# Performance work log

Hardware: AMD Instinct MI355X
Metric: run time of the kernel (lower is better)

The kernel has to match this reference:

```python
import jax, jax.numpy as jnp
import numpy as np

H = 32  # rnn/encoder/residual hidden dim
NEG = -1e9


def gru(x, h0, Wih, Whh, bih, bhh):
    # x: (B,T,D), h0: (B,H); torch GRU gate order [r,z,n]
    xp = jnp.swapaxes(x @ Wih.T + bih, 0, 1)  # (T,B,3H)

    def step(h, xt):
        gh = h @ Whh.T + bhh
        xr, xz, xn = jnp.split(xt, 3, axis=-1)
        hr, hz, hn = jnp.split(gh, 3, axis=-1)
        r = jax.nn.sigmoid(xr + hr)
        z = jax.nn.sigmoid(xz + hz)
        n = jnp.tanh(xn + r * hn)
        h_new = (1.0 - z) * n + z * h
        return h_new, h_new

    hT, ys = jax.lax.scan(step, h0, xp)
    return jnp.swapaxes(ys, 0, 1), hT  # (B,T,H), (B,H)


def setup_inputs():
    key = jax.random.key(0)
    ks = jax.random.split(key, 30)
    B, T = 2048, 128
    def lin(k, o, i):
        return jax.random.normal(k, (o, i), jnp.float32) / np.sqrt(i)
    inp = {}
    inp['obs'] = jax.random.normal(ks[0], (B, T, 15), jnp.float32)
    inp['rnn_state'] = jax.random.normal(ks[1], (1, B, 3 * H), jnp.float32)
    inp['enc_air_W'] = lin(ks[2], H, 7); inp['enc_air_b'] = jnp.zeros((H,), jnp.float32)
    inp['enc_m_W'] = lin(ks[3], H, 4); inp['enc_m_b'] = jnp.zeros((H,), jnp.float32)
    inp['air_Wih'] = lin(ks[4], 3 * H, H); inp['air_Whh'] = lin(ks[5], 3 * H, H)
    inp['air_bih'] = jnp.zeros((3 * H,), jnp.float32); inp['air_bhh'] = jnp.zeros((3 * H,), jnp.float32)
    inp['m_Wih'] = lin(ks[6], 3 * H, H); inp['m_Whh'] = lin(ks[7], 3 * H, H)
    inp['m_bih'] = jnp.zeros((3 * H,), jnp.float32); inp['m_bhh'] = jnp.zeros((3 * H,), jnp.float32)
    inp['attn_in_w'] = lin(ks[8], 3 * H, H); inp['attn_in_b'] = jnp.zeros((3 * H,), jnp.float32)
    inp['attn_out_w'] = lin(ks[9], H, H); inp['attn_out_b'] = jnp.zeros((H,), jnp.float32)
    inp['mlp_W0'] = lin(ks[10], 256, 2 * H); inp['mlp_b0'] = jnp.zeros((256,), jnp.float32)
    inp['mlp_W1'] = lin(ks[11], 256, 256); inp['mlp_b1'] = jnp.zeros((256,), jnp.float32)
    inp['out_W'] = lin(ks[12], 1, 256); inp['out_b'] = jnp.zeros((1,), jnp.float32)
    return inp


def reference(obs, rnn_state, enc_air_W, enc_air_b, enc_m_W, enc_m_b,
              air_Wih, air_Whh, air_bih, air_bhh,
              m_Wih, m_Whh, m_bih, m_bhh,
              attn_in_w, attn_in_b, attn_out_w, attn_out_b,
              mlp_W0, mlp_b0, mlp_W1, mlp_b1, out_W, out_b):
    B, T, _ = obs.shape
    h_air0 = rnn_state[0, :, :H]                       # (B,H)
    h_m0 = rnn_state[0, :, H:].reshape(2 * B, H)       # faithful reshape (1,B,64)->(1,2B,32)

    # aircraft branch
    air_emb = obs[..., 8:] @ enc_air_W.T + enc_air_b   # (B,T,H)
    air_feat, next_h_air = gru(air_emb, h_air0, air_Wih, air_Whh, air_bih, air_bhh)

    # missile branch: concat missiles along batch dim
    m_raw = jnp.concatenate([obs[..., 0:4], obs[..., 4:8]], axis=0)  # (2B,T,4)
    m_emb = m_raw @ enc_m_W.T + enc_m_b
    m_feat, next_h_m = gru(m_emb, h_m0, m_Wih, m_Whh, m_bih, m_bhh)
    m1_feat, m2_feat = m_feat[:B], m_feat[B:]

    # inactive-missile mask from raw obs
    obs_flat = obs.reshape(-1, 15)
    inact = jnp.array([1.0, 0.0, 1.0, 0.0], jnp.float32)
    mask = jnp.stack([
        jnp.all(jnp.isclose(obs_flat[:, 0:4], inact), axis=-1),
        jnp.all(jnp.isclose(obs_flat[:, 4:8], inact), axis=-1),
    ], axis=1)                                          # (N,2) True = masked

    N = B * T
    air_flat = air_feat.reshape(N, H)
    m1_flat = m1_feat.reshape(N, H)
    m2_flat = m2_feat.reshape(N, H)

    # 2-head attention, q len 1, kv len 2
    Wq, Wk, Wv = jnp.split(attn_in_w, 3, axis=0)
    bq, bk, bv = jnp.split(attn_in_b, 3, axis=0)
    nh, hd = 2, H // 2
    qh = (air_flat @ Wq.T + bq).reshape(N, nh, hd)
    kv = jnp.stack([m1_flat, m2_flat], axis=1)          # (N,2,H)
    kh = (kv @ Wk.T + bk).reshape(N, 2, nh, hd)
    vh = (kv @ Wv.T + bv).reshape(N, 2, nh, hd)
    scores = jnp.einsum('nhd,nkhd->nhk', qh, kh) / np.sqrt(hd)
    scores = scores + jnp.where(mask[:, None, :], NEG, 0.0)
    w = jax.nn.softmax(scores, axis=-1)
    ctx = jnp.einsum('nhk,nkhd->nhd', w, vh).reshape(N, H)
    attn = ctx @ attn_out_w.T + attn_out_b
    attn = jnp.where(jnp.all(mask, axis=-1, keepdims=True), 0.0, attn)  # torch nan_to_num(all-masked)

    fusion = jnp.concatenate([air_flat, attn], axis=-1)  # (N,2H)
    h1 = jax.nn.leaky_relu(fusion @ mlp_W0.T + mlp_b0, 0.01)
    h2 = jax.nn.leaky_relu(h1 @ mlp_W1.T + mlp_b1, 0.01)
    val = h2 @ out_W.T + out_b                           # (N,1)

    next_h = jnp.concatenate([next_h_air, next_h_m.reshape(B, 2 * H)], axis=-1)[None]  # (1,B,96)
    return val, next_h
```

## Files before the change

kernel.cpp:

```cpp
#include <hip/hip_runtime.h>
#include <hip/hip_bf16.h>

#define BB 2048
#define TT 128
#define NN (BB*TT)
#define NVAL NN

#define OFF_W0P   2048u
#define OFF_W1P   10240u
#define OFF_WQKV  43008u
#define OFF_WO    44544u
#define OFF_PWHA  49792u
#define OFF_PWHM  51328u
#define OFF_PWCA  52864u
#define OFF_PWCM  54400u
#define OFF_BHNA  55936u
#define OFF_BHNM  55968u
#define OFF_AIRF  83968u
#define OFF_MF    4278272u
#define OFF_MASK  12666880u

typedef __attribute__((ext_vector_type(8))) short short8;
typedef __attribute__((ext_vector_type(4))) float f32x4;
typedef _Float16 f16x8 __attribute__((ext_vector_type(8)));
typedef unsigned u32x4 __attribute__((ext_vector_type(4)));

__device__ __forceinline__ unsigned short f2bf(float f) {
    unsigned u = __builtin_bit_cast(unsigned, f);
    u += 0x7FFFu + ((u >> 16) & 1u);
    return (unsigned short)(u >> 16);
}
__device__ __forceinline__ unsigned f2h(float f) {
    _Float16 h = (_Float16)f;
    return (unsigned)__builtin_bit_cast(unsigned short, h);
}
__device__ __forceinline__ unsigned pkh2(float a, float b) {
    return (f2h(b) << 16) | f2h(a);
}
__device__ __forceinline__ float fast_rcp(float x) {
    return __builtin_amdgcn_rcpf(x);
}
__device__ __forceinline__ unsigned cvt_pk_bf16(float a, float b) {
    unsigned r;
    asm("v_cvt_pk_bf16_f32 %0, %1, %2" : "=v"(r) : "v"(a), "v"(b));
    return r;
}
__device__ __forceinline__ f32x4 mfma16f(f16x8 a, f16x8 b, f32x4 c) {
    return __builtin_amdgcn_mfma_f32_16x16x32_f16(a, b, c, 0, 0, 0);
}

__global__ __launch_bounds__(256) void prep_kernel(
    const float* __restrict__ enc_air_W, const float* __restrict__ enc_air_b,
    const float* __restrict__ enc_m_W,   const float* __restrict__ enc_m_b,
    const float* __restrict__ air_Wih,   const float* __restrict__ air_bih,
    const float* __restrict__ m_Wih,     const float* __restrict__ m_bih,
    const float* __restrict__ air_Whh,   const float* __restrict__ m_Whh,
    const float* __restrict__ air_bhh,   const float* __restrict__ m_bhh,
    const float* __restrict__ W0,        const float* __restrict__ W1,
    const float* __restrict__ attn_in_w, const float* __restrict__ attn_out_w,
    float* __restrict__ ws)
{
    int b = blockIdx.x, t = threadIdx.x;
    if (b == 0) {
    } else if (b <= 32) {
        unsigned short* w1p = (unsigned short*)(ws + OFF_W1P);
        int base = ((b-1)*256 + t);
        int lane = base & 63;
        int ctf  = base >> 6;
        int ct   = ctf & 15, s = ctf >> 4;
        int col = lane & 15, quad = lane >> 4;
        int k0 = s*32 + quad*8;
        int o  = ct*16 + col;
        #pragma unroll
        for (int j = 0; j < 8; j++)
            w1p[base*8 + j] = f2bf(W1[o*256 + k0 + j]);
    } else if (b <= 40) {
        unsigned short* w0p = (unsigned short*)(ws + OFF_W0P);
        int base = ((b-33)*256 + t);
        int lane = base & 63;
        int ctf  = base >> 6;
        int ct   = ctf & 15, s = ctf >> 4;
        int col = lane & 15, quad = lane >> 4;
        int k0 = s*32 + quad*8;
        int o  = ct*16 + col;
        #pragma unroll
        for (int j = 0; j < 8; j++)
            w0p[base*8 + j] = f2bf(W0[o*64 + k0 + j]);
    } else if (b == 41) {
        unsigned short* wqkv = (unsigned short*)(ws + OFF_WQKV);
        unsigned short* wop  = (unsigned short*)(ws + OFF_WO);
        for (int slot = t; slot < 512; slot += 256) {
            if (slot < 384) {
                int ct = slot >> 6, lane = slot & 63;
                int col = lane & 15, quad = lane >> 4;
                int o = ct*16 + col;
                #pragma unroll
                for (int j = 0; j < 8; j++)
                    wqkv[slot*8 + j] = f2bf(attn_in_w[o*32 + quad*8 + j]);
            } else {
                int s2 = slot - 384;
                int ct = s2 >> 6, lane = s2 & 63;
                int col = lane & 15, quad = lane >> 4;
                #pragma unroll
                for (int j = 0; j < 8; j++)
                    wop[s2*8 + j] = f2bf(attn_out_w[(ct*16+col)*32 + quad*8 + j]);
            }
        }
    } else if (b == 42) {
        unsigned* pa = (unsigned*)(ws + OFF_PWHA);
        unsigned* pm = (unsigned*)(ws + OFF_PWHM);
        for (int s = t; s < 3072; s += 256) {
            int s2 = (s < 1536) ? s : s - 1536;
            const float* W = (s < 1536) ? air_Whh : m_Whh;
            unsigned* dst = (s < 1536) ? pa : pm;
            int tile = s2 >> 8;
            int l    = (s2 >> 2) & 63;
            int d    = s2 & 3;
            int gate = tile >> 1, hfp = tile & 1;
            int rr = l & 15;
            int f  = (rr >> 2)*8 + hfp*4 + (rr & 3);
            int k  = (l >> 4)*8 + d*2;
            int row = gate*32 + f;
            dst[s2] = pkh2(W[row*32 + k], W[row*32 + k + 1]);
        }
    } else {
        unsigned* pa = (unsigned*)(ws + OFF_PWCA);
        unsigned* pm = (unsigned*)(ws + OFF_PWCM);
        for (int s = t; s < 3072; s += 256) {
            bool isA = (s < 1536);
            int s2 = isA ? s : s - 1536;
            unsigned* dst = isA ? pa : pm;
            int tile = s2 >> 8, l = (s2 >> 2) & 63, d = s2 & 3;
            int gate = tile >> 1, hfp = tile & 1;
            int rr = l & 15;
            int f = (rr >> 2)*8 + hfp*4 + (rr & 3);
            int o = gate*32 + f;
            int kb = (l >> 4)*8 + d*2;
            int ni = isA ? 7 : 4;
            float v[2];
            #pragma unroll
            for (int e = 0; e < 2; e++) {
                int k = kb + e;
                float acc = 0.f;
                if (k < ni) {
                    for (int m = 0; m < 32; m++)
                        acc += isA ? air_Wih[o*32+m]*enc_air_W[m*7+k]
                                   : m_Wih[o*32+m]*enc_m_W[m*4+k];
                } else if (k == ni) {
                    acc = isA ? air_bih[o] : m_bih[o];
                    for (int m = 0; m < 32; m++)
                        acc += isA ? air_Wih[o*32+m]*enc_air_b[m]
                                   : m_Wih[o*32+m]*enc_m_b[m];
                    if (gate < 2) acc += isA ? air_bhh[o] : m_bhh[o];
                }
                v[e] = acc;
            }
            dst[s2] = pkh2(v[0], v[1]);
        }
        if (t < 32) {
            ws[OFF_BHNA + t] = air_bhh[64 + t];
            ws[OFF_BHNM + t] = m_bhh[64 + t];
        }
    }
}

template<bool AIRT>
__device__ __forceinline__ void gru_tile(
    const float* __restrict__ obs, const float* __restrict__ rnn,
    const float* __restrict__ ws,
    unsigned short* __restrict__ feat, float* __restrict__ mask_f,
    float* __restrict__ nh_out, int tileIdx)
{
    const int lane = threadIdx.x & 63;
    const int col = lane & 15, quad = lane >> 4;
    const bool q0 = (quad == 0);

    const unsigned* pw = (const unsigned*)(ws + (AIRT ? OFF_PWHA : OFF_PWHM));
    const unsigned* pc = (const unsigned*)(ws + (AIRT ? OFF_PWCA : OFF_PWCM));
    f16x8 whf[6], wcf[6];
    #pragma unroll
    for (int i6 = 0; i6 < 6; i6++) {
        whf[i6] = __builtin_bit_cast(f16x8, *(const u32x4*)(pw + i6*256 + lane*4));
        wcf[i6] = __builtin_bit_cast(f16x8, *(const u32x4*)(pc + i6*256 + lane*4));
    }
    const float* bhnp = ws + (AIRT ? OFF_BHNA : OFF_BHNM) + quad*8;
    f32x4 bhn0 = *(const f32x4*)(bhnp);
    f32x4 bhn1 = *(const f32x4*)(bhnp + 4);

    int hbase, brow = 0, slot = 0;
    size_t featOff;
    const float* xptr;
    if (AIRT) {
        int r = tileIdx*16 + col;
        hbase = r*96;
        featOff = (size_t)r*(TT*32);
        xptr = obs + (size_t)r*(TT*15) + 8;
    } else {
        int i = tileIdx*16 + col;
        slot = (i >= BB) ? 1 : 0;
        brow = i - slot*BB;
        hbase = (i >> 1)*96 + 32 + (i & 1)*32;
        featOff = (size_t)i*(TT*32);
        xptr = obs + (size_t)brow*(TT*15) + slot*4;
    }
    unsigned short* featp = feat + featOff + quad*8;

    f32x4 h0v = *(const f32x4*)(rnn + hbase + quad*8);
    f32x4 h1v = *(const f32x4*)(rnn + hbase + quad*8 + 4);

    constexpr int NI = AIRT ? 7 : 4;
    float nx[NI];
    #pragma unroll
    for (int u = 0; u < NI; u++) nx[u] = xptr[u];

    #pragma unroll 1
    for (int t = 0; t < TT; t++) {
        float cx[NI];
        #pragma unroll
        for (int u = 0; u < NI; u++) cx[u] = nx[u];
        const int tn = (t < TT-1) ? (t+1)*15 : t*15;
        #pragma unroll
        for (int u = 0; u < NI; u++) nx[u] = xptr[tn + u];

        if (!AIRT) {
            bool ok = (fabsf(cx[0] - 1.f) <= 1.00001e-5f) &&
                      (fabsf(cx[1])       <= 1e-8f) &&
                      (fabsf(cx[2] - 1.f) <= 1.00001e-5f) &&
                      (fabsf(cx[3])       <= 1e-8f);
            if (q0) mask_f[((size_t)brow*TT + t)*2 + slot] = ok ? 1.f : 0.f;
        }

        unsigned xd0, xd1, xd2, xd3;
        if (AIRT) {
            xd0 = pkh2(cx[0], cx[1]); xd1 = pkh2(cx[2], cx[3]);
            xd2 = pkh2(cx[4], cx[5]); xd3 = pkh2(cx[6], 1.0f);
        } else {
            xd0 = pkh2(cx[0], cx[1]); xd1 = pkh2(cx[2], cx[3]);
            xd2 = 0x00003C00u;        xd3 = 0u;
        }
        u32x4 xdv;
        xdv[0] = q0 ? xd0 : 0u; xdv[1] = q0 ? xd1 : 0u;
        xdv[2] = q0 ? xd2 : 0u; xdv[3] = q0 ? xd3 : 0u;
        f16x8 xf = __builtin_bit_cast(f16x8, xdv);

        u32x4 hdv;
        hdv[0] = pkh2(h0v[0], h0v[1]); hdv[1] = pkh2(h0v[2], h0v[3]);
        hdv[2] = pkh2(h1v[0], h1v[1]); hdv[3] = pkh2(h1v[2], h1v[3]);
        f16x8 hff = __builtin_bit_cast(f16x8, hdv);

        const f32x4 z4 = {0.f, 0.f, 0.f, 0.f};
        f32x4 aR0 = mfma16f(whf[0], hff, mfma16f(wcf[0], xf, z4));
        f32x4 aR1 = mfma16f(whf[1], hff, mfma16f(wcf[1], xf, z4));
        f32x4 aZ0 = mfma16f(whf[2], hff, mfma16f(wcf[2], xf, z4));
        f32x4 aZ1 = mfma16f(whf[3], hff, mfma16f(wcf[3], xf, z4));
        f32x4 aXN0 = mfma16f(wcf[4], xf, z4);
        f32x4 aXN1 = mfma16f(wcf[5], xf, z4);
        f32x4 aHN0 = mfma16f(whf[4], hff, z4);
        f32x4 aHN1 = mfma16f(whf[5], hff, z4);

        #pragma unroll
        for (int s = 0; s < 4; s++) {
            {
                float r  = fast_rcp(1.f + __expf(-aR0[s]));
                float z  = fast_rcp(1.f + __expf(-aZ0[s]));
                float hn = aHN0[s] + bhn0[s];
                float pre = aXN0[s] + r*hn;
                float e2 = __expf(2.f*pre);
                float n  = 1.f - 2.f*fast_rcp(e2 + 1.f);
                h0v[s] = n + z*(h0v[s] - n);
            }
            {
                float r  = fast_rcp(1.f + __expf(-aR1[s]));
                float z  = fast_rcp(1.f + __expf(-aZ1[s]));
                float hn = aHN1[s] + bhn1[s];
                float pre = aXN1[s] + r*hn;
                float e2 = __expf(2.f*pre);
                float n  = 1.f - 2.f*fast_rcp(e2 + 1.f);
                h1v[s] = n + z*(h1v[s] - n);
            }
        }

        u32x4 fw;
        fw[0] = cvt_pk_bf16(h0v[0], h0v[1]); fw[1] = cvt_pk_bf16(h0v[2], h0v[3]);
        fw[2] = cvt_pk_bf16(h1v[0], h1v[1]); fw[3] = cvt_pk_bf16(h1v[2], h1v[3]);
        *(u32x4*)(featp + (size_t)t*32) = fw;
    }
    *(f32x4*)(nh_out + hbase + quad*8)     = h0v;
    *(f32x4*)(nh_out + hbase + quad*8 + 4) = h1v;
}

__global__ __launch_bounds__(64) void gru_kernel(
    const float* __restrict__ obs, const float* __restrict__ rnn,
    const float* __restrict__ ws,
    unsigned short* __restrict__ air_feat, unsigned short* __restrict__ m_feat,
    float* __restrict__ mask_f, float* __restrict__ nh_out)
{
    int g = blockIdx.x;
    if (g < 128) gru_tile<true >(obs, rnn, ws, air_feat, mask_f, nh_out, g);
    else         gru_tile<false>(obs, rnn, ws, m_feat,  mask_f, nh_out, g - 128);
}

__global__ __launch_bounds__(256) void fused_kernel(
    const unsigned short* __restrict__ air_feat, const unsigned short* __restrict__ m_feat,
    const float* __restrict__ mask_f,
    const unsigned short* __restrict__ wqkv, const float* __restrict__ attn_in_b,
    const unsigned short* __restrict__ wop,  const float* __restrict__ attn_out_b,
    const unsigned short* __restrict__ w0p, const float* __restrict__ b0,
    const unsigned short* __restrict__ w1p, const float* __restrict__ b1,
    const float* __restrict__ outW, const float* __restrict__ outb,
    float* __restrict__ val)
{
    __shared__ unsigned short A1[64*72];
    __shared__ unsigned short U[64*264];
    __shared__ float MS[128];
    __shared__ float PS[4][64];

    unsigned short* AM = U;
    unsigned short* CT = U + 64*72;
    unsigned short* A2 = U;

    const int tid  = threadIdx.x;
    const int lane = tid & 63;
    const int strip = tid >> 6;
    const int col  = lane & 15;
    const int quad = lane >> 4;
    const size_t n0 = (size_t)blockIdx.x * 64;

    short8 wqf[2], wkf[2], wvf[2], wof[2];
    #pragma unroll
    for (int ct = 0; ct < 2; ct++) {
        wqf[ct] = *(const short8*)(wqkv + ((0+ct)*64 + lane)*8);
        wkf[ct] = *(const short8*)(wqkv + ((2+ct)*64 + lane)*8);
        wvf[ct] = *(const short8*)(wqkv + ((4+ct)*64 + lane)*8);
        wof[ct] = *(const short8*)(wop + (ct*64 + lane)*8);
    }

    {
        int row = tid >> 2, c0 = (tid & 3)*8;
        short8 va  = *(const short8*)(air_feat + (n0 + row)*32 + c0);
        *(short8*)&A1[row*72 + c0] = va;
        short8 vm1 = *(const short8*)(m_feat + (n0 + row)*32 + c0);
        *(short8*)&AM[row*72 + c0] = vm1;
        short8 vm2 = *(const short8*)(m_feat + ((size_t)NN + n0 + row)*32 + c0);
        *(short8*)&AM[row*72 + 32 + c0] = vm2;
        if (tid < 128) MS[tid] = mask_f[n0*2 + tid];
    }
    __syncthreads();

    {
        short8 a_air = *(const short8*)&A1[(strip*16 + col)*72 + quad*8];
        short8 a_m1  = *(const short8*)&AM[(strip*16 + col)*72 + quad*8];
        short8 a_m2  = *(const short8*)&AM[(strip*16 + col)*72 + 32 + quad*8];

        f32x4 q[2], k1[2], k2[2], v1[2], v2[2], ao[2];
        #pragma unroll
        for (int ct = 0; ct < 2; ct++) {
            f32x4 z = (f32x4){0.f,0.f,0.f,0.f};
            q[ct]  = __builtin_amdgcn_mfma_f32_16x16x32_bf16(a_air, wqf[ct], z, 0,0,0);
            k1[ct] = __builtin_amdgcn_mfma_f32_16x16x32_bf16(a_m1,  wkf[ct], z, 0,0,0);
            k2[ct] = __builtin_amdgcn_mfma_f32_16x16x32_bf16(a_m2,  wkf[ct], z, 0,0,0);
            v1[ct] = __builtin_amdgcn_mfma_f32_16x16x32_bf16(a_m1,  wvf[ct], z, 0,0,0);
            v2[ct] = __builtin_amdgcn_mfma_f32_16x16x32_bf16(a_m2,  wvf[ct], z, 0,0,0);
        }
        float bqr[2], bkr[2], bvr[2];
        #pragma unroll
        for (int ct = 0; ct < 2; ct++) {
            bqr[ct] = attn_in_b[ct*16 + col];
            bkr[ct] = attn_in_b[32 + ct*16 + col];
            bvr[ct] = attn_in_b[64 + ct*16 + col];
        }
        float p1s[2][4], p2s[2][4];
        #pragma unroll
        for (int ct = 0; ct < 2; ct++) {
            #pragma unroll
            for (int reg = 0; reg < 4; reg++) {
                float qq = q[ct][reg] + bqr[ct];
                float p1 = qq * (k1[ct][reg] + bkr[ct]);
                float p2 = qq * (k2[ct][reg] + bkr[ct]);
                #pragma unroll
                for (int m = 1; m < 16; m <<= 1) {
                    p1 += __shfl_xor(p1, m, 64);
                    p2 += __shfl_xor(p2, m, 64);
                }
                p1s[ct][reg] = p1; p2s[ct][reg] = p2;
            }
        }
        float bothm[4];
        #pragma unroll
        for (int reg = 0; reg < 4; reg++) {
            int rloc = strip*16 + quad*4 + reg;
            float m0v = MS[rloc*2], m1v = MS[rloc*2 + 1];
            bothm[reg] = (m0v > 0.5f && m1v > 0.5f) ? 1.f : 0.f;
            #pragma unroll
            for (int ct = 0; ct < 2; ct++) {
                float s1 = p1s[ct][reg]*0.25f + (m0v > 0.5f ? -1e9f : 0.f);
                float s2 = p2s[ct][reg]*0.25f + (m1v > 0.5f ? -1e9f : 0.f);
                float mx = fmaxf(s1, s2);
                float e1 = __expf(s1 - mx), e2 = __expf(s2 - mx);
                float inv = fast_rcp(e1 + e2);
                float ctxv = ((v1[ct][reg] + bvr[ct])*e1 +
                              (v2[ct][reg] + bvr[ct])*e2) * inv;
                CT[rloc*40 + ct*16 + col] = f2bf(ctxv);
            }
        }
        short8 a_ctx = *(const short8*)&CT[(strip*16 + col)*40 + quad*8];
        #pragma unroll
        for (int ct = 0; ct < 2; ct++) {
            f32x4 z = (f32x4){0.f,0.f,0.f,0.f};
            ao[ct] = __builtin_amdgcn_mfma_f32_16x16x32_bf16(a_ctx, wof[ct], z, 0,0,0);
        }
        float bor[2] = { attn_out_b[col], attn_out_b[16 + col] };
        #pragma unroll
        for (int reg = 0; reg < 4; reg++) {
            int rloc = strip*16 + quad*4 + reg;
            #pragma unroll
            for (int ct = 0; ct < 2; ct++) {
                float av = ao[ct][reg] + bor[ct];
                av = (bothm[reg] > 0.5f) ? 0.f : av;
                A1[rloc*72 + 32 + ct*16 + col] = f2bf(av);
            }
        }
    }
    __syncthreads();

    float b0r[4], b1r[4], owr[4];
    #pragma unroll
    for (int c = 0; c < 4; c++) {
        int ct = strip*4 + c;
        b0r[c] = b0[ct*16 + col];
        b1r[c] = b1[ct*16 + col];
        owr[c] = outW[ct*16 + col];
    }
    const float outb0 = outb[0];

    f32x4 acc1[4][4];
    #pragma unroll
    for (int s = 0; s < 4; s++)
        #pragma unroll
        for (int c = 0; c < 4; c++) acc1[s][c] = (f32x4){0.f,0.f,0.f,0.f};
    {
        short8 bfr[4], nbfr[4];
        #pragma unroll
        for (int c = 0; c < 4; c++)
            bfr[c] = *(const short8*)(w0p + ((0*16 + strip*4 + c)*64 + lane)*8);
        #pragma unroll
        for (int ks = 0; ks < 2; ks++) {
            if (ks < 1) {
                #pragma unroll
                for (int c = 0; c < 4; c++)
                    nbfr[c] = *(const short8*)(w0p + (((ks+1)*16 + strip*4 + c)*64 + lane)*8);
            }
            short8 a[4];
            #pragma unroll
            for (int s = 0; s < 4; s++)
                a[s] = *(const short8*)&A1[(s*16 + col)*72 + ks*32 + quad*8];
            #pragma unroll
            for (int c = 0; c < 4; c++)
                #pragma unroll
                for (int s = 0; s < 4; s++)
                    acc1[s][c] = __builtin_amdgcn_mfma_f32_16x16x32_bf16(a[s], bfr[c], acc1[s][c], 0, 0, 0);
            #pragma unroll
            for (int c = 0; c < 4; c++) bfr[c] = nbfr[c];
        }
    }
    __syncthreads();
    #pragma unroll
    for (int s = 0; s < 4; s++) {
        #pragma unroll
        for (int c = 0; c < 4; c++) {
            int ct = strip*4 + c;
            #pragma unroll
            for (int reg = 0; reg < 4; reg++) {
                float h = acc1[s][c][reg] + b0r[c];
                h = (h > 0.f) ? h : 0.01f*h;
                A2[(s*16 + quad*4 + reg)*264 + ct*16 + col] = f2bf(h);
            }
        }
    }
    __syncthreads();

    f32x4 acc2[4][4];
    #pragma unroll
    for (int s = 0; s < 4; s++)
        #pragma unroll
        for (int c = 0; c < 4; c++) acc2[s][c] = (f32x4){0.f,0.f,0.f,0.f};
    {
        short8 bfr[4], nbfr[4];
        #pragma unroll
        for (int c = 0; c < 4; c++)
            bfr[c] = *(const short8*)(w1p + ((0*16 + strip*4 + c)*64 + lane)*8);
        #pragma unroll
        for (int ks = 0; ks < 8; ks++) {
            if (ks < 7) {
                #pragma unroll
                for (int c = 0; c < 4; c++)
                    nbfr[c] = *(const short8*)(w1p + (((ks+1)*16 + strip*4 + c)*64 + lane)*8);
            }
            short8 a[4];
            #pragma unroll
            for (int s = 0; s < 4; s++)
                a[s] = *(const short8*)&A2[(s*16 + col)*264 + ks*32 + quad*8];
            #pragma unroll
            for (int c = 0; c < 4; c++)
                #pragma unroll
                for (int s = 0; s < 4; s++)
                    acc2[s][c] = __builtin_amdgcn_mfma_f32_16x16x32_bf16(a[s], bfr[c], acc2[s][c], 0, 0, 0);
            #pragma unroll
            for (int c = 0; c < 4; c++) bfr[c] = nbfr[c];
        }
    }

    #pragma unroll
    for (int s = 0; s < 4; s++) {
        float pv[4];
        #pragma unroll
        for (int reg = 0; reg < 4; reg++) pv[reg] = 0.f;
        #pragma unroll
        for (int c = 0; c < 4; c++) {
            #pragma unroll
            for (int reg = 0; reg < 4; reg++) {
                float h = acc2[s][c][reg] + b1r[c];
                h = (h > 0.f) ? h : 0.01f*h;
                pv[reg] += h*owr[c];
            }
        }
        #pragma unroll
        for (int reg = 0; reg < 4; reg++) {
            #pragma unroll
            for (int m = 1; m < 16; m <<= 1)
                pv[reg] += __shfl_xor(pv[reg], m, 64);
            if (col == 0) PS[strip][s*16 + quad*4 + reg] = pv[reg];
        }
    }
    __syncthreads();
    if (tid < 64)
        val[n0 + tid] = PS[0][tid] + PS[1][tid] + PS[2][tid] + PS[3][tid] + outb0;
}

extern "C" void kernel_launch(void* const* d_in, const int* in_sizes, int n_in,
                              void* d_out, int out_size, void* d_ws, size_t ws_size,
                              hipStream_t stream) {
    const float* obs        = (const float*)d_in[0];
    const float* rnn        = (const float*)d_in[1];
    const float* enc_air_W  = (const float*)d_in[2];
    const float* enc_air_b  = (const float*)d_in[3];
    const float* enc_m_W    = (const float*)d_in[4];
    const float* enc_m_b    = (const float*)d_in[5];
    const float* air_Wih    = (const float*)d_in[6];
    const float* air_Whh    = (const float*)d_in[7];
    const float* air_bih    = (const float*)d_in[8];
    const float* air_bhh    = (const float*)d_in[9];
    const float* m_Wih      = (const float*)d_in[10];
    const float* m_Whh      = (const float*)d_in[11];
    const float* m_bih      = (const float*)d_in[12];
    const float* m_bhh      = (const float*)d_in[13];
    const float* attn_in_w  = (const float*)d_in[14];
    const float* attn_in_b  = (const float*)d_in[15];
    const float* attn_out_w = (const float*)d_in[16];
    const float* attn_out_b = (const float*)d_in[17];
    const float* mlp_W0     = (const float*)d_in[18];
    const float* mlp_b0     = (const float*)d_in[19];
    const float* mlp_W1     = (const float*)d_in[20];
    const float* mlp_b1     = (const float*)d_in[21];
    const float* out_W      = (const float*)d_in[22];
    const float* out_b      = (const float*)d_in[23];

    float* ws  = (float*)d_ws;
    float* out = (float*)d_out;

    prep_kernel<<<44, 256, 0, stream>>>(enc_air_W, enc_air_b, enc_m_W, enc_m_b,
                                        air_Wih, air_bih, m_Wih, m_bih,
                                        air_Whh, m_Whh, air_bhh, m_bhh,
                                        mlp_W0, mlp_W1, attn_in_w, attn_out_w, ws);

    gru_kernel<<<384, 64, 0, stream>>>(obs, rnn, ws,
                                       (unsigned short*)(ws + OFF_AIRF),
                                       (unsigned short*)(ws + OFF_MF),
                                       ws + OFF_MASK, out + NVAL);

    fused_kernel<<<NN/64, 256, 0, stream>>>((const unsigned short*)(ws + OFF_AIRF),
                                            (const unsigned short*)(ws + OFF_MF),
                                            ws + OFF_MASK,
                                            (const unsigned short*)(ws + OFF_WQKV), attn_in_b,
                                            (const unsigned short*)(ws + OFF_WO),   attn_out_b,
                                            (const unsigned short*)(ws + OFF_W0P), mlp_b0,
                                            (const unsigned short*)(ws + OFF_W1P), mlp_b1,
                                            out_W, out_b, out);
}
```

Baseline: 352.5 us.

## Prefetch per-tile GRU inputs into LDS before the recurrent loop

Before the sequential time loop, each GRU block now loads its whole tile of observation inputs (16 rows × 128 steps), converts them to packed fp16 MFMA operands and computes the mask, writing into a swizzled shared-memory buffer. The recurrent loop then reads one 16-byte LDS entry per step instead of issuing strided global loads and repacking every step. This takes the global-memory latency and the conversion work off the serial critical path. The cost is a prologue that is not overlapped with compute and about 32 KB of LDS per block.

```diff
diff --git a/kernel.cpp b/kernel.cpp
--- a/kernel.cpp
+++ b/kernel.cpp
@@ -169,7 +169,7 @@
     const float* __restrict__ obs, const float* __restrict__ rnn,
     const float* __restrict__ ws,
     unsigned short* __restrict__ feat, float* __restrict__ mask_f,
-    float* __restrict__ nh_out, int tileIdx)
+    float* __restrict__ nh_out, int tileIdx, unsigned* __restrict__ XH)
 {
     const int lane = threadIdx.x & 63;
     const int col = lane & 15, quad = lane >> 4;
@@ -187,61 +187,56 @@
     f32x4 bhn0 = *(const f32x4*)(bhnp);
     f32x4 bhn1 = *(const f32x4*)(bhnp + 4);
 
-    int hbase, brow = 0, slot = 0;
-    size_t featOff;
-    const float* xptr;
-    if (AIRT) {
-        int r = tileIdx*16 + col;
-        hbase = r*96;
-        featOff = (size_t)r*(TT*32);
-        xptr = obs + (size_t)r*(TT*15) + 8;
-    } else {
-        int i = tileIdx*16 + col;
-        slot = (i >= BB) ? 1 : 0;
-        brow = i - slot*BB;
-        hbase = (i >> 1)*96 + 32 + (i & 1)*32;
-        featOff = (size_t)i*(TT*32);
-        xptr = obs + (size_t)brow*(TT*15) + slot*4;
-    }
+    int slot = 0, tb;
+    if (AIRT) { tb = tileIdx*16; }
+    else      { slot = tileIdx >> 7; tb = (tileIdx & 127)*16; }
+
+    {
+        const int coff = AIRT ? 8 : slot*4;
+        #pragma unroll 8
+        for (int it = 0; it < 32; it++) {
+            int s = it*64 + lane;
+            int r = s >> 7, t = s & 127;
+            const float* p = obs + (size_t)(tb + r)*1920 + t*15 + coff;
+            unsigned d0, d1, d2, d3;
+            if (AIRT) {
+                d0 = pkh2(p[0], p[1]); d1 = pkh2(p[2], p[3]);
+                d2 = pkh2(p[4], p[5]); d3 = pkh2(p[6], 1.0f);
+            } else {
+                float x0 = p[0], x1 = p[1], x2 = p[2], x3 = p[3];
+                d0 = pkh2(x0, x1); d1 = pkh2(x2, x3);
+                d2 = 0x00003C00u; d3 = 0u;
+                bool ok = (fabsf(x0 - 1.f) <= 1.00001e-5f) && (fabsf(x1) <= 1e-8f) &&
+                          (fabsf(x2 - 1.f) <= 1.00001e-5f) && (fabsf(x3) <= 1e-8f);
+                mask_f[((size_t)(tb + r)*TT + t)*2 + slot] = ok ? 1.f : 0.f;
+            }
+            unsigned off = (unsigned)(r*512 + 4*(t ^ (r & 7)));
+            *(u32x4*)(XH + off) = (u32x4){d0, d1, d2, d3};
+        }
+        if (lane == 0) *(u32x4*)(XH + 8192) = (u32x4){0u, 0u, 0u, 0u};
+    }
+    __syncthreads();
+
+    int rowi = tileIdx*16 + col;
+    int hbase;
+    size_t featOff = (size_t)rowi*(TT*32);
+    if (AIRT) hbase = rowi*96;
+    else      hbase = (rowi >> 1)*96 + 32 + (rowi & 1)*32;
     unsigned short* featp = feat + featOff + quad*8;
 
     f32x4 h0v = *(const f32x4*)(rnn + hbase + quad*8);
     f32x4 h1v = *(const f32x4*)(rnn + hbase + quad*8 + 4);
 
-    constexpr int NI = AIRT ? 7 : 4;
-    float nx[NI];
-    #pragma unroll
-    for (int u = 0; u < NI; u++) nx[u] = xptr[u];
+    const int xk = col & 7;
+    const unsigned bidx = (unsigned)col*512;
+    u32x4 xc = *(const u32x4*)(XH + (q0 ? bidx + 4u*(unsigned)(0 ^ xk) : 8192u));
 
     #pragma unroll 1
     for (int t = 0; t < TT; t++) {
-        float cx[NI];
-        #pragma unroll
-        for (int u = 0; u < NI; u++) cx[u] = nx[u];
-        const int tn = (t < TT-1) ? (t+1)*15 : t*15;
-        #pragma unroll
-        for (int u = 0; u < NI; u++) nx[u] = xptr[tn + u];
-
-        if (!AIRT) {
-            bool ok = (fabsf(cx[0] - 1.f) <= 1.00001e-5f) &&
-                      (fabsf(cx[1])       <= 1e-8f) &&
-                      (fabsf(cx[2] - 1.f) <= 1.00001e-5f) &&
-                      (fabsf(cx[3])       <= 1e-8f);
-            if (q0) mask_f[((size_t)brow*TT + t)*2 + slot] = ok ? 1.f : 0.f;
-        }
-
-        unsigned xd0, xd1, xd2, xd3;
-        if (AIRT) {
-            xd0 = pkh2(cx[0], cx[1]); xd1 = pkh2(cx[2], cx[3]);
-            xd2 = pkh2(cx[4], cx[5]); xd3 = pkh2(cx[6], 1.0f);
-        } else {
-            xd0 = pkh2(cx[0], cx[1]); xd1 = pkh2(cx[2], cx[3]);
-            xd2 = 0x00003C00u;        xd3 = 0u;
-        }
-        u32x4 xdv;
-        xdv[0] = q0 ? xd0 : 0u; xdv[1] = q0 ? xd1 : 0u;
-        xdv[2] = q0 ? xd2 : 0u; xdv[3] = q0 ? xd3 : 0u;
-        f16x8 xf = __builtin_bit_cast(f16x8, xdv);
+        const int tn = (t < TT-1) ? t+1 : t;
+        u32x4 xnv = *(const u32x4*)(XH + (q0 ? bidx + 4u*(unsigned)(tn ^ xk) : 8192u));
+
+        f16x8 xf = __builtin_bit_cast(f16x8, xc);
 
         u32x4 hdv;
         hdv[0] = pkh2(h0v[0], h0v[1]); hdv[1] = pkh2(h0v[2], h0v[3]);
@@ -284,20 +279,23 @@
         fw[0] = cvt_pk_bf16(h0v[0], h0v[1]); fw[1] = cvt_pk_bf16(h0v[2], h0v[3]);
         fw[2] = cvt_pk_bf16(h1v[0], h1v[1]); fw[3] = cvt_pk_bf16(h1v[2], h1v[3]);
         *(u32x4*)(featp + (size_t)t*32) = fw;
+
+        xc = xnv;
     }
     *(f32x4*)(nh_out + hbase + quad*8)     = h0v;
     *(f32x4*)(nh_out + hbase + quad*8 + 4) = h1v;
 }
 
-__global__ __launch_bounds__(64) void gru_kernel(
+__global__ __launch_bounds__(64, 1) void gru_kernel(
     const float* __restrict__ obs, const float* __restrict__ rnn,
     const float* __restrict__ ws,
     unsigned short* __restrict__ air_feat, unsigned short* __restrict__ m_feat,
     float* __restrict__ mask_f, float* __restrict__ nh_out)
 {
+    __shared__ unsigned XH[8196];
     int g = blockIdx.x;
-    if (g < 128) gru_tile<true >(obs, rnn, ws, air_feat, mask_f, nh_out, g);
-    else         gru_tile<false>(obs, rnn, ws, m_feat,  mask_f, nh_out, g - 128);
+    if (g < 128) gru_tile<true >(obs, rnn, ws, air_feat, mask_f, nh_out, g, XH);
+    else         gru_tile<false>(obs, rnn, ws, m_feat,  mask_f, nh_out, g - 128, XH);
 }
 
 __global__ __launch_bounds__(256) void fused_kernel(
```

Result: faster. 320.9 us (-9.0%).
